# Kernel optimization log

Measured on AMD Instinct MI355X. Metric: run time of the kernel, lower is better.

Reference implementation:

```python
import jax, jax.numpy as jnp
import numpy as np

E, D, B, P = 16, 5, 8, 65536
EXPERT_DIM = 128
N_BETAS = 4
EPS = 1e-6


def setup_inputs() -> dict:
    key = jax.random.key(0)
    k1, k2, k3, k4 = jax.random.split(key, 4)
    V = jax.random.normal(k1, (E, D, B, P), dtype=jnp.float32)
    masks = jax.random.randint(k2, (E, P), 0, 2) > 0  # bool [E, P]
    betas = jax.random.normal(k3, (E, N_BETAS), dtype=jnp.float32)
    expert_pos_embed = jax.random.normal(k4, (E, EXPERT_DIM), dtype=jnp.float32)
    temperature = jnp.ones((1,), dtype=jnp.float32)
    return {
        'V': V,
        'masks': masks,
        'betas': betas,
        'expert_pos_embed': expert_pos_embed,
        'temperature': temperature,
        'num_patches': P,
    }


def reference(V, masks, betas, expert_pos_embed, temperature, num_patches):
    # per-expert scalar weights
    pos_w = jax.nn.sigmoid(expert_pos_embed.mean(axis=1))          # [E]
    beta_w = 1.0 + jax.nn.sigmoid(betas).mean(axis=1)              # [E] (sum(sigmoid)/len)
    w = pos_w * beta_w                                             # [E]

    m = masks.astype(V.dtype)                                      # [E, P]
    # masked weighted vote accumulation over experts, per direction
    num = jnp.einsum('e,edbp,ep->dbp', w, V, m)                    # [D, B, P]
    den = jnp.einsum('e,ep->p', w, m)                              # [P] (same for all d, b)
    den = jnp.maximum(den, EPS)

    patch_votes = (num / den[None, None, :]).sum(axis=0) / 5.0     # [B, P]
    return patch_votes / jnp.abs(temperature[0])
```

## Files before the change

kernel.cpp:

```cpp
#include <hip/hip_runtime.h>
#include <math.h>

#define NE 16
#define ND 5
#define NB 8
#define NP 65536
#define EDIM 128
#define NBETAS 4


__global__ __launch_bounds__(256, 4) void cfa_fused(
    const float* __restrict__ V,
    const void* __restrict__ masks,
    const float* __restrict__ betas,
    const float* __restrict__ embed,
    const float* __restrict__ temp,
    float* __restrict__ out)
{
    __shared__ float sw[NE];
    __shared__ float sscale;
    __shared__ int   sflag;
    __shared__ float4 redA[128];
    __shared__ float4 redD[128];

    const int tid = threadIdx.x;

    if (tid < 128) {
        const int e = tid >> 3, j = tid & 7;
        const float4* ep = (const float4*)(embed + e * EDIM + j * 16);
        float s = 0.f;
        #pragma unroll
        for (int i = 0; i < 4; ++i) { float4 v = ep[i]; s += v.x + v.y + v.z + v.w; }
        s += __shfl_xor(s, 4, 64);
        s += __shfl_xor(s, 2, 64);
        s += __shfl_xor(s, 1, 64);
        if (j == 0) {
            float pos_w = 1.f / (1.f + __expf(-s * (1.f / EDIM)));
            float bs = 0.f;
            #pragma unroll
            for (int i = 0; i < NBETAS; ++i)
                bs += 1.f / (1.f + __expf(-betas[e * NBETAS + i]));
            sw[e] = pos_w * (1.f + bs * (1.f / NBETAS));
        }
        if (tid == 0) sscale = 0.2f / fabsf(temp[0]);
    } else if (tid >= 192) {
        const int lane = tid - 192;
        unsigned x = ((const unsigned*)masks)[lane];
        unsigned o1 = x & 0x0000FF00u, o3 = x & 0xFF000000u;
        #pragma unroll
        for (int off = 32; off; off >>= 1) {
            o1 |= __shfl_xor(o1, off, 64);
            o3 |= __shfl_xor(o3, off, 64);
        }
        if (lane == 0) sflag = o1 ? 0 : (o3 ? 2 : 1);
    }
    __syncthreads();

    const int q  = blockIdx.x * 128 + (tid & 127);
    const int b  = q >> 14;
    const int p  = (q & 16383) << 2;
    const int e0 = (tid >> 7) << 3;
    const int flag = sflag;

    float4 wm[8];
    if (flag == 0) {
        const unsigned char* mb = (const unsigned char*)masks + p;
        #pragma unroll
        for (int ee = 0; ee < 8; ++ee) {
            uchar4 u = *(const uchar4*)(mb + (e0 + ee) * NP);
            const float we = sw[e0 + ee];
            wm[ee].x = we * (float)u.x; wm[ee].y = we * (float)u.y;
            wm[ee].z = we * (float)u.z; wm[ee].w = we * (float)u.w;
        }
    } else if (flag == 1) {
        const int* mi = (const int*)masks + p;
        #pragma unroll
        for (int ee = 0; ee < 8; ++ee) {
            int4 u = *(const int4*)(mi + (e0 + ee) * NP);
            const float we = sw[e0 + ee];
            wm[ee].x = we * (float)u.x; wm[ee].y = we * (float)u.y;
            wm[ee].z = we * (float)u.z; wm[ee].w = we * (float)u.w;
        }
    } else {
        const float* mf = (const float*)masks + p;
        #pragma unroll
        for (int ee = 0; ee < 8; ++ee) {
            float4 u = *(const float4*)(mf + (e0 + ee) * NP);
            const float we = sw[e0 + ee];
            wm[ee].x = we * u.x; wm[ee].y = we * u.y;
            wm[ee].z = we * u.z; wm[ee].w = we * u.w;
        }
    }

    float4 den = {0.f, 0.f, 0.f, 0.f};
    #pragma unroll
    for (int ee = 0; ee < 8; ++ee) {
        den.x += wm[ee].x; den.y += wm[ee].y; den.z += wm[ee].z; den.w += wm[ee].w;
    }

    float4 a = {0.f, 0.f, 0.f, 0.f};
    const float* vb = V + b * NP + p;
    #pragma unroll
    for (int ee = 0; ee < 8; ++ee) {
        const float* ve = vb + (e0 + ee) * (ND * NB * NP);
        #pragma unroll
        for (int d = 0; d < ND; ++d) {
            float4 v = *(const float4*)(ve + d * (NB * NP));
            a.x = fmaf(wm[ee].x, v.x, a.x);
            a.y = fmaf(wm[ee].y, v.y, a.y);
            a.z = fmaf(wm[ee].z, v.z, a.z);
            a.w = fmaf(wm[ee].w, v.w, a.w);
        }
    }

    if (tid >= 128) {
        redA[tid - 128] = a;
        redD[tid - 128] = den;
    }
    __syncthreads();
    if (tid < 128) {
        float4 a2 = redA[tid], d2 = redD[tid];
        a.x += a2.x; a.y += a2.y; a.z += a2.z; a.w += a2.w;
        den.x += d2.x; den.y += d2.y; den.z += d2.z; den.w += d2.w;
        const float scale = sscale;
        float4 o;
        o.x = a.x / fmaxf(den.x, 1e-6f) * scale;
        o.y = a.y / fmaxf(den.y, 1e-6f) * scale;
        o.z = a.z / fmaxf(den.z, 1e-6f) * scale;
        o.w = a.w / fmaxf(den.w, 1e-6f) * scale;
        *(float4*)(out + b * NP + p) = o;
    }
}

extern "C" void kernel_launch(void* const* d_in, const int* in_sizes, int n_in,
                              void* d_out, int out_size, void* d_ws, size_t ws_size,
                              hipStream_t stream) {
    const float* V     = (const float*)d_in[0];
    const void*  masks = d_in[1];
    const float* betas = (const float*)d_in[2];
    const float* embed = (const float*)d_in[3];
    const float* temp  = (const float*)d_in[4];

    float* out = (float*)d_out;

    const int blocks = (NB * NP / 4) / 128;
    cfa_fused<<<blocks, 256, 0, stream>>>(V, masks, betas, embed, temp, out);
}
```

Baseline: 33.16 us.

## Compute expert weights per wavefront and prefetch V before weight setup

Drops the shared-memory prologue and its __syncthreads. Every wavefront now recomputes the 16 expert weights and the mask-dtype flag itself using shuffles. The first expert's five V loads are issued before that setup so they overlap the weight computation. All V loads use nontemporal hints to avoid polluting the cache with streamed data. The cost is redundant per-wave work on the embedding and betas and higher register pressure from the prefetched values.

After: 33.24 us. About the same (+0.2%).

```diff
diff --git a/kernel.cpp b/kernel.cpp
--- a/kernel.cpp
+++ b/kernel.cpp
@@ -8,6 +8,8 @@
 #define EDIM 128
 #define NBETAS 4
 
+typedef float f32x4 __attribute__((ext_vector_type(4)));
+
 
 __global__ __launch_bounds__(256, 4) void cfa_fused(
     const float* __restrict__ V,
@@ -17,118 +19,124 @@
     const float* __restrict__ temp,
     float* __restrict__ out)
 {
-    __shared__ float sw[NE];
-    __shared__ float sscale;
-    __shared__ int   sflag;
     __shared__ float4 redA[128];
     __shared__ float4 redD[128];
 
-    const int tid = threadIdx.x;
-
-    if (tid < 128) {
-        const int e = tid >> 3, j = tid & 7;
-        const float4* ep = (const float4*)(embed + e * EDIM + j * 16);
-        float s = 0.f;
-        #pragma unroll
-        for (int i = 0; i < 4; ++i) { float4 v = ep[i]; s += v.x + v.y + v.z + v.w; }
-        s += __shfl_xor(s, 4, 64);
-        s += __shfl_xor(s, 2, 64);
-        s += __shfl_xor(s, 1, 64);
-        if (j == 0) {
-            float pos_w = 1.f / (1.f + __expf(-s * (1.f / EDIM)));
-            float bs = 0.f;
-            #pragma unroll
-            for (int i = 0; i < NBETAS; ++i)
-                bs += 1.f / (1.f + __expf(-betas[e * NBETAS + i]));
-            sw[e] = pos_w * (1.f + bs * (1.f / NBETAS));
-        }
-        if (tid == 0) sscale = 0.2f / fabsf(temp[0]);
-    } else if (tid >= 192) {
-        const int lane = tid - 192;
-        unsigned x = ((const unsigned*)masks)[lane];
-        unsigned o1 = x & 0x0000FF00u, o3 = x & 0xFF000000u;
-        #pragma unroll
-        for (int off = 32; off; off >>= 1) {
-            o1 |= __shfl_xor(o1, off, 64);
-            o3 |= __shfl_xor(o3, off, 64);
-        }
-        if (lane == 0) sflag = o1 ? 0 : (o3 ? 2 : 1);
-    }
-    __syncthreads();
+    const int tid  = threadIdx.x;
+    const int lane = tid & 63;
 
     const int q  = blockIdx.x * 128 + (tid & 127);
     const int b  = q >> 14;
     const int p  = (q & 16383) << 2;
     const int e0 = (tid >> 7) << 3;
-    const int flag = sflag;
 
-    float4 wm[8];
-    if (flag == 0) {
-        const unsigned char* mb = (const unsigned char*)masks + p;
+    const float* vb  = V + b * NP + p;
+    const float* ve0 = vb + e0 * (ND * NB * NP);
+    f32x4 pre[ND];
+    #pragma unroll
+    for (int d = 0; d < ND; ++d)
+        pre[d] = __builtin_nontemporal_load((const f32x4*)(ve0 + d * (NB * NP)));
+
+    unsigned mx = ((const unsigned*)masks)[lane];
+    unsigned o1 = mx & 0x0000FF00u, o3 = mx & 0xFF000000u;
+    #pragma unroll
+    for (int off = 32; off; off >>= 1) {
+        o1 |= __shfl_xor(o1, off, 64);
+        o3 |= __shfl_xor(o3, off, 64);
+    }
+    const int flag = o1 ? 0 : (o3 ? 2 : 1);
+
+    {
+        const int e = lane >> 2, r = lane & 3;
+        const float4* ep = (const float4*)(embed + e * EDIM + r * 32);
+        float s = 0.f;
+        #pragma unroll
+        for (int i = 0; i < 8; ++i) { float4 v = ep[i]; s += v.x + v.y + v.z + v.w; }
+        s += __shfl_xor(s, 1, 64);
+        s += __shfl_xor(s, 2, 64);
+        float bsig = 1.f / (1.f + __expf(-betas[e * NBETAS + r]));
+        bsig += __shfl_xor(bsig, 1, 64);
+        bsig += __shfl_xor(bsig, 2, 64);
+        float pos_w = 1.f / (1.f + __expf(-s * (1.f / EDIM)));
+        float wfull = pos_w * (1.f + bsig * (1.f / NBETAS));
+        float wv[8];
+        #pragma unroll
+        for (int ee = 0; ee < 8; ++ee)
+            wv[ee] = __shfl(wfull, (e0 + ee) << 2, 64);
+
+        const float scale = 0.2f / fabsf(temp[0]);
+
+        float4 wm[8];
+        if (flag == 0) {
+            const unsigned char* mb = (const unsigned char*)masks + p;
+            #pragma unroll
+            for (int ee = 0; ee < 8; ++ee) {
+                uchar4 u = *(const uchar4*)(mb + (e0 + ee) * NP);
+                wm[ee].x = wv[ee] * (float)u.x; wm[ee].y = wv[ee] * (float)u.y;
+                wm[ee].z = wv[ee] * (float)u.z; wm[ee].w = wv[ee] * (float)u.w;
+            }
+        } else if (flag == 1) {
+            const int* mi = (const int*)masks + p;
+            #pragma unroll
+            for (int ee = 0; ee < 8; ++ee) {
+                int4 u = *(const int4*)(mi + (e0 + ee) * NP);
+                wm[ee].x = wv[ee] * (float)u.x; wm[ee].y = wv[ee] * (float)u.y;
+                wm[ee].z = wv[ee] * (float)u.z; wm[ee].w = wv[ee] * (float)u.w;
+            }
+        } else {
+            const float* mf = (const float*)masks + p;
+            #pragma unroll
+            for (int ee = 0; ee < 8; ++ee) {
+                float4 u = *(const float4*)(mf + (e0 + ee) * NP);
+                wm[ee].x = wv[ee] * u.x; wm[ee].y = wv[ee] * u.y;
+                wm[ee].z = wv[ee] * u.z; wm[ee].w = wv[ee] * u.w;
+            }
+        }
+
+        float4 den = {0.f, 0.f, 0.f, 0.f};
         #pragma unroll
         for (int ee = 0; ee < 8; ++ee) {
-            uchar4 u = *(const uchar4*)(mb + (e0 + ee) * NP);
-            const float we = sw[e0 + ee];
-            wm[ee].x = we * (float)u.x; wm[ee].y = we * (float)u.y;
-            wm[ee].z = we * (float)u.z; wm[ee].w = we * (float)u.w;
+            den.x += wm[ee].x; den.y += wm[ee].y;
+            den.z += wm[ee].z; den.w += wm[ee].w;
         }
-    } else if (flag == 1) {
-        const int* mi = (const int*)masks + p;
-        #pragma unroll
-        for (int ee = 0; ee < 8; ++ee) {
-            int4 u = *(const int4*)(mi + (e0 + ee) * NP);
-            const float we = sw[e0 + ee];
-            wm[ee].x = we * (float)u.x; wm[ee].y = we * (float)u.y;
-            wm[ee].z = we * (float)u.z; wm[ee].w = we * (float)u.w;
-        }
-    } else {
-        const float* mf = (const float*)masks + p;
-        #pragma unroll
-        for (int ee = 0; ee < 8; ++ee) {
-            float4 u = *(const float4*)(mf + (e0 + ee) * NP);
-            const float we = sw[e0 + ee];
-            wm[ee].x = we * u.x; wm[ee].y = we * u.y;
-            wm[ee].z = we * u.z; wm[ee].w = we * u.w;
-        }
-    }
 
-    float4 den = {0.f, 0.f, 0.f, 0.f};
-    #pragma unroll
-    for (int ee = 0; ee < 8; ++ee) {
-        den.x += wm[ee].x; den.y += wm[ee].y; den.z += wm[ee].z; den.w += wm[ee].w;
-    }
-
-    float4 a = {0.f, 0.f, 0.f, 0.f};
-    const float* vb = V + b * NP + p;
-    #pragma unroll
-    for (int ee = 0; ee < 8; ++ee) {
-        const float* ve = vb + (e0 + ee) * (ND * NB * NP);
+        float4 a = {0.f, 0.f, 0.f, 0.f};
         #pragma unroll
         for (int d = 0; d < ND; ++d) {
-            float4 v = *(const float4*)(ve + d * (NB * NP));
-            a.x = fmaf(wm[ee].x, v.x, a.x);
-            a.y = fmaf(wm[ee].y, v.y, a.y);
-            a.z = fmaf(wm[ee].z, v.z, a.z);
-            a.w = fmaf(wm[ee].w, v.w, a.w);
+            a.x = fmaf(wm[0].x, pre[d].x, a.x);
+            a.y = fmaf(wm[0].y, pre[d].y, a.y);
+            a.z = fmaf(wm[0].z, pre[d].z, a.z);
+            a.w = fmaf(wm[0].w, pre[d].w, a.w);
         }
-    }
+        #pragma unroll
+        for (int ee = 1; ee < 8; ++ee) {
+            const float* ve = vb + (e0 + ee) * (ND * NB * NP);
+            #pragma unroll
+            for (int d = 0; d < ND; ++d) {
+                f32x4 v = __builtin_nontemporal_load((const f32x4*)(ve + d * (NB * NP)));
+                a.x = fmaf(wm[ee].x, v.x, a.x);
+                a.y = fmaf(wm[ee].y, v.y, a.y);
+                a.z = fmaf(wm[ee].z, v.z, a.z);
+                a.w = fmaf(wm[ee].w, v.w, a.w);
+            }
+        }
 
-    if (tid >= 128) {
-        redA[tid - 128] = a;
-        redD[tid - 128] = den;
-    }
-    __syncthreads();
-    if (tid < 128) {
-        float4 a2 = redA[tid], d2 = redD[tid];
-        a.x += a2.x; a.y += a2.y; a.z += a2.z; a.w += a2.w;
-        den.x += d2.x; den.y += d2.y; den.z += d2.z; den.w += d2.w;
-        const float scale = sscale;
-        float4 o;
-        o.x = a.x / fmaxf(den.x, 1e-6f) * scale;
-        o.y = a.y / fmaxf(den.y, 1e-6f) * scale;
-        o.z = a.z / fmaxf(den.z, 1e-6f) * scale;
-        o.w = a.w / fmaxf(den.w, 1e-6f) * scale;
-        *(float4*)(out + b * NP + p) = o;
+        if (tid >= 128) {
+            redA[tid - 128] = a;
+            redD[tid - 128] = den;
+        }
+        __syncthreads();
+        if (tid < 128) {
+            float4 a2 = redA[tid], d2 = redD[tid];
+            a.x += a2.x; a.y += a2.y; a.z += a2.z; a.w += a2.w;
+            den.x += d2.x; den.y += d2.y; den.z += d2.z; den.w += d2.w;
+            float4 o;
+            o.x = a.x / fmaxf(den.x, 1e-6f) * scale;
+            o.y = a.y / fmaxf(den.y, 1e-6f) * scale;
+            o.z = a.z / fmaxf(den.z, 1e-6f) * scale;
+            o.w = a.w / fmaxf(den.w, 1e-6f) * scale;
+            *(float4*)(out + b * NP + p) = o;
+        }
     }
 }
 
```
